# Kernel tuning notes

Measured on AMD Instinct MI355X. Metric: run time of the kernel, lower is better.

Reference implementation:

```python
import jax, jax.numpy as jnp
import numpy as np

N_NODES = 50000
N_EDGES = 800000
IN_C, HID_C, LAT_C = 128, 64, 32
DEC_HID, REC_C = 64, 128


def _glorot(key, shape):
    fan_in, fan_out = shape
    lim = jnp.sqrt(6.0 / (fan_in + fan_out))
    return jax.random.uniform(key, shape, jnp.float32, -lim, lim)


def setup_inputs() -> dict:
    key = jax.random.key(0)
    ks = jax.random.split(key, 8)
    x = jax.random.normal(ks[0], (N_NODES, IN_C), jnp.float32)
    edge_index = jax.random.randint(ks[1], (2, N_EDGES), 0, N_NODES, jnp.int64 if jax.config.jax_enable_x64 else jnp.int32)
    return {
        "x": x,
        "edge_index": edge_index,
        "W_e1": _glorot(ks[2], (IN_C, HID_C)), "b_e1": jnp.zeros((HID_C,), jnp.float32),
        "W_e2": _glorot(ks[3], (HID_C, LAT_C)), "b_e2": jnp.zeros((LAT_C,), jnp.float32),
        "W_d1": _glorot(ks[4], (LAT_C, DEC_HID)), "b_d1": jnp.zeros((DEC_HID,), jnp.float32),
        "W_d2": _glorot(ks[5], (DEC_HID, REC_C)), "b_d2": jnp.zeros((REC_C,), jnp.float32),
    }


def _gcn_conv(x, src, dst, dinv, W, b, n_nodes):
    # GCNConv: h = D^{-1/2} (A + I) D^{-1/2} (x W) + b, expressed over the edge list
    h = x @ W                                   # [N, out]
    norm = dinv[src] * dinv[dst]                # [E+N] symmetric normalization
    msg = h[src] * norm[:, None]                # gather + per-edge scale (memory-bound)
    out = jax.ops.segment_sum(msg, dst, num_segments=n_nodes)  # scatter-add
    return out + b


def reference(x, edge_index, W_e1, b_e1, W_e2, b_e2, W_d1, b_d1, W_d2, b_d2):
    n = x.shape[0]
    loops = jnp.arange(n, dtype=edge_index.dtype)
    src = jnp.concatenate([edge_index[0], loops])
    dst = jnp.concatenate([edge_index[1], loops])
    # degree (with self-loops) computed once; deg >= 1 so rsqrt is safe
    deg = jax.ops.segment_sum(jnp.ones_like(src, dtype=x.dtype), dst, num_segments=n)
    dinv = jax.lax.rsqrt(deg)

    # encoder (dropout is eval-mode identity)
    h = jax.nn.relu(_gcn_conv(x, src, dst, dinv, W_e1, b_e1, n))
    z = _gcn_conv(h, src, dst, dinv, W_e2, b_e2, n)           # latent embeddings
    # decoder mirrors GCNConv layers
    d = jax.nn.relu(_gcn_conv(z, src, dst, dinv, W_d1, b_d1, n))
    x_rec = _gcn_conv(d, src, dst, dinv, W_d2, b_d2, n)       # [N, reconstructed_feature_dim]
    return x_rec
```

## Files before the change

kernel.cpp:

```cpp
#include <hip/hip_runtime.h>

typedef _Float16 half4 __attribute__((ext_vector_type(4)));


static constexpr int NPB_SHIFT = 6;
static constexpr int NPB = 1 << NPB_SHIFT;
static constexpr int MAX_BKT = 1024;
static constexpr int PS_CHUNK = 4096;

__global__ __launch_bounds__(256) void hist_kernel(const int* __restrict__ dst, int E,
                                                   int nbkt, int* __restrict__ hist) {
    __shared__ int lc[MAX_BKT];
    int tid = threadIdx.x;
    int b = blockIdx.x;
    int e0 = b * PS_CHUNK;
    int e1 = e0 + PS_CHUNK; if (e1 > E) e1 = E;
    for (int i = tid; i < nbkt; i += 256) lc[i] = 0;
    __syncthreads();
    for (int i = e0 + tid; i < e1; i += 256)
        atomicAdd(&lc[dst[i] >> NPB_SHIFT], 1);
    __syncthreads();
    for (int i = tid; i < nbkt; i += 256) hist[(size_t)b * nbkt + i] = lc[i];
}

__global__ __launch_bounds__(256) void col_scan_kernel(int* __restrict__ hist, int nchunk,
                                                       int nbkt, int* __restrict__ bcnt) {
    int i = blockIdx.x * 4 + (threadIdx.x >> 6);
    if (i >= nbkt) return;
    int lane = threadIdx.x & 63;
    int run = 0;
    for (int c0 = 0; c0 < nchunk; c0 += 64) {
        int c = c0 + lane;
        int v = (c < nchunk) ? hist[(size_t)c * nbkt + i] : 0;
        int inc = v;
#pragma unroll
        for (int m = 1; m < 64; m <<= 1) {
            int u = __shfl_up(inc, m);
            if (lane >= m) inc += u;
        }
        if (c < nchunk) hist[(size_t)c * nbkt + i] = run + inc - v;
        run += __shfl(inc, 63);
    }
    if (lane == 0) bcnt[i] = run;
}

__global__ __launch_bounds__(256) void bucket_scan_kernel(const int* __restrict__ bcnt, int nbkt,
                                                          int* __restrict__ bbase,
                                                          int* __restrict__ rowp, int n) {
    __shared__ int wsum[4];
    int tid = threadIdx.x, lane = tid & 63, w = tid >> 6;
    int chunk = (nbkt + 255) / 256;
    int begin = tid * chunk;
    int end = begin + chunk; if (end > nbkt) end = nbkt;
    int s = 0;
    for (int i = begin; i < end; ++i) s += bcnt[i];
    int inc = s;
#pragma unroll
    for (int m = 1; m < 64; m <<= 1) {
        int u = __shfl_up(inc, m);
        if (lane >= m) inc += u;
    }
    if (lane == 63) wsum[w] = inc;
    __syncthreads();
    int off = 0;
    for (int i = 0; i < w; ++i) off += wsum[i];
    int run = off + inc - s;
    for (int i = begin; i < end; ++i) {
        bbase[i] = run;
        run += bcnt[i];
    }
    if (tid == 255) { bbase[nbkt] = run; rowp[n] = run; }
}

__global__ __launch_bounds__(256) void pair_blocksort_kernel(const int* __restrict__ src,
                                                             const int* __restrict__ dst,
                                                             int E, int nbkt,
                                                             const int* __restrict__ hist,
                                                             const int* __restrict__ bbase,
                                                             int2* __restrict__ part) {
    __shared__ int2 pairs[PS_CHUNK];
    __shared__ int lbase[MAX_BKT];
    __shared__ int lcur[MAX_BKT];
    __shared__ int gpos[MAX_BKT];
    __shared__ int wsum[4];
    const int tid = threadIdx.x;
    const int b = blockIdx.x;
    const int e0 = b * PS_CHUNK;
    int e1 = e0 + PS_CHUNK; if (e1 > E) e1 = E;

    for (int i = tid; i < nbkt; i += 256) {
        lcur[i] = 0;
        gpos[i] = bbase[i] + hist[(size_t)b * nbkt + i];
    }
    __syncthreads();
    for (int i = e0 + tid; i < e1; i += 256)
        atomicAdd(&lcur[dst[i] >> NPB_SHIFT], 1);
    __syncthreads();
    {
        int b0 = tid * 4;
        int v[4]; int s = 0;
#pragma unroll
        for (int k = 0; k < 4; ++k) {
            int bb = b0 + k;
            v[k] = (bb < nbkt) ? lcur[bb] : 0;
            s += v[k];
        }
        int lane = tid & 63, w = tid >> 6;
        int inc = s;
#pragma unroll
        for (int m = 1; m < 64; m <<= 1) {
            int u = __shfl_up(inc, m);
            if (lane >= m) inc += u;
        }
        if (lane == 63) wsum[w] = inc;
        __syncthreads();
        int off = 0;
        for (int i = 0; i < w; ++i) off += wsum[i];
        int run = off + inc - s;
        __syncthreads();
#pragma unroll
        for (int k = 0; k < 4; ++k) {
            int bb = b0 + k;
            if (bb < nbkt) { lbase[bb] = run; lcur[bb] = run; }
            run += v[k];
        }
    }
    __syncthreads();
    for (int i = e0 + tid; i < e1; i += 256) {
        int s = src[i], d = dst[i];
        int p = atomicAdd(&lcur[d >> NPB_SHIFT], 1);
        pairs[p] = make_int2(s, d);
    }
    __syncthreads();
    const int cnt = e1 - e0;
    for (int i = tid; i < cnt; i += 256) {
        int2 pr = pairs[i];
        int bk = pr.y >> NPB_SHIFT;
        part[gpos[bk] + (i - lbase[bk])] = pr;
    }
}

__global__ __launch_bounds__(256) void bucket_csr_kernel(const int2* __restrict__ part,
                                                         const int* __restrict__ bbase, int n,
                                                         int* __restrict__ rowp,
                                                         float* __restrict__ dinv,
                                                         int* __restrict__ csr) {
    __shared__ int lcnt[NPB];
    int b = blockIdx.x, tid = threadIdx.x;
    int node0 = b << NPB_SHIFT;
    int nloc = n - node0; if (nloc > NPB) nloc = NPB;
    int p0 = bbase[b], p1 = bbase[b + 1];
    if (tid < NPB) lcnt[tid] = 0;
    __syncthreads();
    for (int i = p0 + tid; i < p1; i += 256)
        atomicAdd(&lcnt[part[i].y & (NPB - 1)], 1);
    __syncthreads();
    if (tid < 64) {
        int c = lcnt[tid];
        int inc = c;
#pragma unroll
        for (int m = 1; m < 64; m <<= 1) {
            int u = __shfl_up(inc, m);
            if (tid >= m) inc += u;
        }
        int base = p0 + inc - c;
        if (tid < nloc) {
            rowp[node0 + tid] = base;
            dinv[node0 + tid] = rsqrtf((float)(c + 1));
        }
        lcnt[tid] = base;
    }
    __syncthreads();
    for (int i = p0 + tid; i < p1; i += 256) {
        int2 pr = part[i];
        int pos = atomicAdd(&lcnt[pr.y & (NPB - 1)], 1);
        csr[pos] = pr.x;
    }
}


template <bool HALF>
__device__ __forceinline__ float4 ldrow4(const void* H, size_t off) {
    if constexpr (HALF) {
        half4 h = *reinterpret_cast<const half4*>(reinterpret_cast<const _Float16*>(H) + off);
        return make_float4((float)h.x, (float)h.y, (float)h.z, (float)h.w);
    } else {
        return *reinterpret_cast<const float4*>(reinterpret_cast<const float*>(H) + off);
    }
}

template <bool HALF>
__device__ __forceinline__ void strow4(void* H, size_t off, float4 o) {
    if constexpr (HALF) {
        half4 hv;
        hv.x = (_Float16)o.x; hv.y = (_Float16)o.y;
        hv.z = (_Float16)o.z; hv.w = (_Float16)o.w;
        *reinterpret_cast<half4*>(reinterpret_cast<_Float16*>(H) + off) = hv;
    } else {
        *reinterpret_cast<float4*>(reinterpret_cast<float*>(H) + off) = o;
    }
}

template <int K, int OUT, int BN, bool BIAS, bool RELU, bool SCALE, bool HALF_IN, bool HALF_OUT>
__global__ __launch_bounds__(16 * (BN / 4)) void gemm_tile_kernel(
        const void* __restrict__ X, const float* __restrict__ W,
        const float* __restrict__ bias, const float* __restrict__ dinv,
        void* __restrict__ Hout, int n) {
    constexpr int BM = 64;
    constexpr int KB = (K > 64) ? 64 : K;
    constexpr int NTHR = 16 * (BN / 4);
    constexpr int KV = KB / 4;

    __shared__ float At[KB][BM + 4];
    __shared__ float Bl[K][BN];

    const int tid = threadIdx.x;
    const int tx = tid % (BN / 4);
    const int ty = tid / (BN / 4);
    const int rb = blockIdx.x * BM;
    const int co = blockIdx.y * BN;

    for (int i = tid; i < K * BN / 4; i += NTHR) {
        int k = i / (BN / 4);
        int c0 = (i % (BN / 4)) * 4;
        *reinterpret_cast<float4*>(&Bl[k][c0]) =
            *reinterpret_cast<const float4*>(&W[(size_t)k * OUT + co + c0]);
    }

    float acc[4][4] = {};

#pragma unroll
    for (int ch = 0; ch < K / KB; ++ch) {
        if (ch) __syncthreads();
        for (int i = tid; i < BM * KV; i += NTHR) {
            int r = i / KV;
            int k0 = (i % KV) * 4;
            int rg = rb + r; if (rg > n - 1) rg = n - 1;
            float4 xv = ldrow4<HALF_IN>(X, (size_t)rg * K + ch * KB + k0);
            At[k0 + 0][r] = xv.x;
            At[k0 + 1][r] = xv.y;
            At[k0 + 2][r] = xv.z;
            At[k0 + 3][r] = xv.w;
        }
        __syncthreads();

#pragma unroll 8
        for (int k = 0; k < KB; ++k) {
            float4 a = *reinterpret_cast<const float4*>(&At[k][ty * 4]);
            float4 b = *reinterpret_cast<const float4*>(&Bl[ch * KB + k][tx * 4]);
            acc[0][0] = fmaf(a.x, b.x, acc[0][0]); acc[0][1] = fmaf(a.x, b.y, acc[0][1]);
            acc[0][2] = fmaf(a.x, b.z, acc[0][2]); acc[0][3] = fmaf(a.x, b.w, acc[0][3]);
            acc[1][0] = fmaf(a.y, b.x, acc[1][0]); acc[1][1] = fmaf(a.y, b.y, acc[1][1]);
            acc[1][2] = fmaf(a.y, b.z, acc[1][2]); acc[1][3] = fmaf(a.y, b.w, acc[1][3]);
            acc[2][0] = fmaf(a.z, b.x, acc[2][0]); acc[2][1] = fmaf(a.z, b.y, acc[2][1]);
            acc[2][2] = fmaf(a.z, b.z, acc[2][2]); acc[2][3] = fmaf(a.z, b.w, acc[2][3]);
            acc[3][0] = fmaf(a.w, b.x, acc[3][0]); acc[3][1] = fmaf(a.w, b.y, acc[3][1]);
            acc[3][2] = fmaf(a.w, b.z, acc[3][2]); acc[3][3] = fmaf(a.w, b.w, acc[3][3]);
        }
    }

    float4 bv = make_float4(0.f, 0.f, 0.f, 0.f);
    if (BIAS) bv = *reinterpret_cast<const float4*>(&bias[co + tx * 4]);
    int r0 = rb + ty * 4;
#pragma unroll
    for (int i = 0; i < 4; ++i) {
        int r = r0 + i;
        if (r < n) {
            float4 o;
            o.x = acc[i][0]; o.y = acc[i][1]; o.z = acc[i][2]; o.w = acc[i][3];
            if (BIAS) { o.x += bv.x; o.y += bv.y; o.z += bv.z; o.w += bv.w; }
            if (RELU) {
                o.x = fmaxf(o.x, 0.f); o.y = fmaxf(o.y, 0.f);
                o.z = fmaxf(o.z, 0.f); o.w = fmaxf(o.w, 0.f);
            }
            if (SCALE) {
                float dv = dinv[r];
                o.x *= dv; o.y *= dv; o.z *= dv; o.w *= dv;
            }
            strow4<HALF_OUT>(Hout, (size_t)r * OUT + co + tx * 4, o);
        }
    }
}

template <int C, bool RELU, bool HAS_BIAS, bool POST_SCALE, bool HALF_IN, bool HALF_OUT>
__global__ __launch_bounds__(256) void aggregate_kernel(const void* __restrict__ H,
                                                        const int* __restrict__ row,
                                                        const int* __restrict__ csr_src,
                                                        const float* __restrict__ dinv,
                                                        const float* __restrict__ bias,
                                                        void* __restrict__ Y, int n) {
    constexpr int LPN = C / 4;
    constexpr int EG = 64 / LPN;
    int wid = (blockIdx.x * blockDim.x + threadIdx.x) >> 6;
    if (wid >= n) return;
    int lane = threadIdx.x & 63;
    int g = lane / LPN;
    int c0 = (lane % LPN) * 4;
    const int node = wid;

    float4 a0 = make_float4(0.f, 0.f, 0.f, 0.f);
    float4 a1 = a0, a2 = a0, a3 = a0;
    if (g == 0) a0 = ldrow4<HALF_IN>(H, (size_t)node * C + c0);
    int e = row[node] + g;
    int end = row[node + 1];
    for (; e + 3 * EG < end; e += 4 * EG) {
        int s0 = csr_src[e];
        int s1 = csr_src[e + EG];
        int s2 = csr_src[e + 2 * EG];
        int s3 = csr_src[e + 3 * EG];
        float4 h0 = ldrow4<HALF_IN>(H, (size_t)s0 * C + c0);
        float4 h1 = ldrow4<HALF_IN>(H, (size_t)s1 * C + c0);
        float4 h2 = ldrow4<HALF_IN>(H, (size_t)s2 * C + c0);
        float4 h3 = ldrow4<HALF_IN>(H, (size_t)s3 * C + c0);
        a0.x += h0.x; a0.y += h0.y; a0.z += h0.z; a0.w += h0.w;
        a1.x += h1.x; a1.y += h1.y; a1.z += h1.z; a1.w += h1.w;
        a2.x += h2.x; a2.y += h2.y; a2.z += h2.z; a2.w += h2.w;
        a3.x += h3.x; a3.y += h3.y; a3.z += h3.z; a3.w += h3.w;
    }
    for (; e < end; e += EG) {
        int s = csr_src[e];
        float4 hv = ldrow4<HALF_IN>(H, (size_t)s * C + c0);
        a0.x += hv.x; a0.y += hv.y; a0.z += hv.z; a0.w += hv.w;
    }
    float4 acc;
    acc.x = (a0.x + a1.x) + (a2.x + a3.x);
    acc.y = (a0.y + a1.y) + (a2.y + a3.y);
    acc.z = (a0.z + a1.z) + (a2.z + a3.z);
    acc.w = (a0.w + a1.w) + (a2.w + a3.w);
#pragma unroll
    for (int m = LPN; m < 64; m <<= 1) {
        acc.x += __shfl_xor(acc.x, m);
        acc.y += __shfl_xor(acc.y, m);
        acc.z += __shfl_xor(acc.z, m);
        acc.w += __shfl_xor(acc.w, m);
    }
    if (g == 0) {
        float dv = dinv[node];
        float4 o;
        o.x = acc.x * dv; o.y = acc.y * dv; o.z = acc.z * dv; o.w = acc.w * dv;
        if (HAS_BIAS) {
            o.x += bias[c0 + 0]; o.y += bias[c0 + 1];
            o.z += bias[c0 + 2]; o.w += bias[c0 + 3];
        }
        if (RELU) {
            o.x = fmaxf(o.x, 0.f); o.y = fmaxf(o.y, 0.f);
            o.z = fmaxf(o.z, 0.f); o.w = fmaxf(o.w, 0.f);
        }
        if (POST_SCALE) { o.x *= dv; o.y *= dv; o.z *= dv; o.w *= dv; }
        strow4<HALF_OUT>(Y, (size_t)node * C + c0, o);
    }
}


static inline int cdiv(int a, int b) { return (a + b - 1) / b; }

extern "C" void kernel_launch(void* const* d_in, const int* in_sizes, int n_in,
                              void* d_out, int out_size, void* d_ws, size_t ws_size,
                              hipStream_t stream) {
    const float* x   = (const float*)d_in[0];
    const int*   ei  = (const int*)d_in[1];
    const float* We1 = (const float*)d_in[2];
    const float* be1 = (const float*)d_in[3];
    const float* We2 = (const float*)d_in[4];
    const float* be2 = (const float*)d_in[5];
    const float* Wd1 = (const float*)d_in[6];
    const float* bd1 = (const float*)d_in[7];
    const float* Wd2 = (const float*)d_in[8];
    const float* bd2 = (const float*)d_in[9];

    const int n = in_sizes[0] / 128;
    const int E = in_sizes[1] / 2;
    const int* src = ei;
    const int* dst = ei + E;
    const int nbkt = cdiv(n, NPB);
    const int nchunk = cdiv(E, PS_CHUNK);
    const int nrb = cdiv(n, 64);
    const int nwv = cdiv(n * 64, 256);

    char* ws = (char*)d_ws;
    auto carve = [&](size_t bytes) -> void* {
        void* p = (void*)ws;
        ws += (bytes + 255) & ~(size_t)255;
        return p;
    };
    int*   hist = (int*)carve((size_t)nchunk * nbkt * 4);
    int*   bcnt = (int*)carve((size_t)nbkt * 4);
    int*   bbase= (int*)carve((size_t)(nbkt + 1) * 4);
    int2*  part = (int2*)carve((size_t)E * 8);
    int*   rowp = (int*)carve((size_t)(n + 1) * 4);
    float* dinv = (float*)carve((size_t)n * 4);
    int*   csr  = (int*)carve((size_t)E * 4);
    void*  bufA = carve((size_t)n * 64 * 4);
    void*  bufB = carve((size_t)n * 64 * 4);
    void*  bufC = carve((size_t)n * 32 * 4);

    hist_kernel<<<nchunk, 256, 0, stream>>>(dst, E, nbkt, hist);
    col_scan_kernel<<<cdiv(nbkt, 4), 256, 0, stream>>>(hist, nchunk, nbkt, bcnt);
    bucket_scan_kernel<<<1, 256, 0, stream>>>(bcnt, nbkt, bbase, rowp, n);
    pair_blocksort_kernel<<<nchunk, 256, 0, stream>>>(src, dst, E, nbkt, hist, bbase, part);
    bucket_csr_kernel<<<nbkt, 256, 0, stream>>>(part, bbase, n, rowp, dinv, csr);

    gemm_tile_kernel<128, 64, 64, false, false, true, false, true>
        <<<dim3(nrb, 1), 256, 0, stream>>>(x, We1, nullptr, dinv, bufA, n);
    aggregate_kernel<64, true, true, false, true, true>
        <<<nwv, 256, 0, stream>>>(bufA, rowp, csr, dinv, be1, bufB, n);

    gemm_tile_kernel<64, 32, 32, false, false, true, true, true>
        <<<dim3(nrb, 1), 128, 0, stream>>>(bufB, We2, nullptr, dinv, bufA, n);
    aggregate_kernel<32, false, true, true, true, true>
        <<<nwv, 256, 0, stream>>>(bufA, rowp, csr, dinv, be2, bufC, n);

    aggregate_kernel<32, false, false, false, true, true>
        <<<nwv, 256, 0, stream>>>(bufC, rowp, csr, dinv, nullptr, bufA, n);
    gemm_tile_kernel<32, 64, 64, true, true, true, true, true>
        <<<dim3(nrb, 1), 256, 0, stream>>>(bufA, Wd1, bd1, dinv, bufB, n);

    aggregate_kernel<64, false, false, false, true, true>
        <<<nwv, 256, 0, stream>>>(bufB, rowp, csr, dinv, nullptr, bufA, n);
    gemm_tile_kernel<64, 128, 64, true, false, false, true, false>
        <<<dim3(nrb, 2), 256, 0, stream>>>(bufA, Wd2, bd2, dinv, d_out, n);
}
```

Baseline: 197.9 us.

## Fuse CSR build with first GEMM and aggregation with following GEMMs

Packs each (src,dst) pair into a single int, which halves the partition buffer. The bucket CSR build is merged with the first-layer GEMM, since a 64-node bucket matches a 64-row GEMM tile. Three aggregate-then-GEMM pairs become one agg_gemm kernel: aggregated rows are staged in fp16 shared memory and multiplied by a shared-memory fp16 copy of W. This removes kernel launches and intermediate global round trips. In exchange, the fused kernels have large shared-memory footprints, which may lower occupancy, and the weights are rounded to fp16.

```diff
diff --git a/kernel.cpp b/kernel.cpp
--- a/kernel.cpp
+++ b/kernel.cpp
@@ -77,7 +77,7 @@
                                                              int E, int nbkt,
                                                              const int* __restrict__ hist,
                                                              const int* __restrict__ bbase,
-                                                             int2* __restrict__ part) {
+                                                             int* __restrict__ part) {
     __shared__ int2 pairs[PS_CHUNK];
     __shared__ int lbase[MAX_BKT];
     __shared__ int lcur[MAX_BKT];
@@ -136,45 +136,7 @@
     for (int i = tid; i < cnt; i += 256) {
         int2 pr = pairs[i];
         int bk = pr.y >> NPB_SHIFT;
-        part[gpos[bk] + (i - lbase[bk])] = pr;
-    }
-}
-
-__global__ __launch_bounds__(256) void bucket_csr_kernel(const int2* __restrict__ part,
-                                                         const int* __restrict__ bbase, int n,
-                                                         int* __restrict__ rowp,
-                                                         float* __restrict__ dinv,
-                                                         int* __restrict__ csr) {
-    __shared__ int lcnt[NPB];
-    int b = blockIdx.x, tid = threadIdx.x;
-    int node0 = b << NPB_SHIFT;
-    int nloc = n - node0; if (nloc > NPB) nloc = NPB;
-    int p0 = bbase[b], p1 = bbase[b + 1];
-    if (tid < NPB) lcnt[tid] = 0;
-    __syncthreads();
-    for (int i = p0 + tid; i < p1; i += 256)
-        atomicAdd(&lcnt[part[i].y & (NPB - 1)], 1);
-    __syncthreads();
-    if (tid < 64) {
-        int c = lcnt[tid];
-        int inc = c;
-#pragma unroll
-        for (int m = 1; m < 64; m <<= 1) {
-            int u = __shfl_up(inc, m);
-            if (tid >= m) inc += u;
-        }
-        int base = p0 + inc - c;
-        if (tid < nloc) {
-            rowp[node0 + tid] = base;
-            dinv[node0 + tid] = rsqrtf((float)(c + 1));
-        }
-        lcnt[tid] = base;
-    }
-    __syncthreads();
-    for (int i = p0 + tid; i < p1; i += 256) {
-        int2 pr = part[i];
-        int pos = atomicAdd(&lcnt[pr.y & (NPB - 1)], 1);
-        csr[pos] = pr.x;
+        part[gpos[bk] + (i - lbase[bk])] = (pr.x << NPB_SHIFT) | (pr.y & (NPB - 1));
     }
 }
 
@@ -201,84 +163,213 @@
     }
 }
 
-template <int K, int OUT, int BN, bool BIAS, bool RELU, bool SCALE, bool HALF_IN, bool HALF_OUT>
-__global__ __launch_bounds__(16 * (BN / 4)) void gemm_tile_kernel(
-        const void* __restrict__ X, const float* __restrict__ W,
-        const float* __restrict__ bias, const float* __restrict__ dinv,
-        void* __restrict__ Hout, int n) {
-    constexpr int BM = 64;
-    constexpr int KB = (K > 64) ? 64 : K;
-    constexpr int NTHR = 16 * (BN / 4);
-    constexpr int KV = KB / 4;
-
-    __shared__ float At[KB][BM + 4];
-    __shared__ float Bl[K][BN];
-
-    const int tid = threadIdx.x;
-    const int tx = tid % (BN / 4);
-    const int ty = tid / (BN / 4);
-    const int rb = blockIdx.x * BM;
-    const int co = blockIdx.y * BN;
-
-    for (int i = tid; i < K * BN / 4; i += NTHR) {
-        int k = i / (BN / 4);
-        int c0 = (i % (BN / 4)) * 4;
-        *reinterpret_cast<float4*>(&Bl[k][c0]) =
-            *reinterpret_cast<const float4*>(&W[(size_t)k * OUT + co + c0]);
+__global__ __launch_bounds__(256) void csr_g1_kernel(
+        const int* __restrict__ part, const int* __restrict__ bbase, int n,
+        int* __restrict__ rowp, float* __restrict__ dinv, int* __restrict__ csr,
+        const float* __restrict__ X, const float* __restrict__ We1,
+        void* __restrict__ H1) {
+    __shared__ int lcnt[NPB];
+    __shared__ float sdinv[NPB];
+    __shared__ __align__(16) char smem[50176];
+    const int b = blockIdx.x, tid = threadIdx.x;
+    const int node0 = b << NPB_SHIFT;
+    int nloc = n - node0; if (nloc > NPB) nloc = NPB;
+    const int p0 = bbase[b], p1 = bbase[b + 1];
+
+    if (tid < NPB) lcnt[tid] = 0;
+    __syncthreads();
+    for (int i = p0 + tid; i < p1; i += 256)
+        atomicAdd(&lcnt[part[i] & (NPB - 1)], 1);
+    __syncthreads();
+    if (tid < 64) {
+        int c = lcnt[tid];
+        int inc = c;
+#pragma unroll
+        for (int m = 1; m < 64; m <<= 1) {
+            int u = __shfl_up(inc, m);
+            if (tid >= m) inc += u;
+        }
+        int base = p0 + inc - c;
+        float dv = rsqrtf((float)(c + 1));
+        if (tid < nloc) {
+            rowp[node0 + tid] = base;
+            dinv[node0 + tid] = dv;
+        }
+        sdinv[tid] = dv;
+        lcnt[tid] = base;
+    }
+    __syncthreads();
+    for (int i = p0 + tid; i < p1; i += 256) {
+        int w = part[i];
+        int pos = atomicAdd(&lcnt[w & (NPB - 1)], 1);
+        csr[pos] = w >> NPB_SHIFT;
+    }
+    __syncthreads();
+
+    float (*At)[68] = reinterpret_cast<float (*)[68]>(smem);
+    float (*Bl)[64] = reinterpret_cast<float (*)[64]>(smem + 17408);
+    const int tx = tid % 16, ty = tid / 16;
+
+    for (int i = tid; i < 128 * 16; i += 256) {
+        int k = i / 16, c4 = (i % 16) * 4;
+        *reinterpret_cast<float4*>(&Bl[k][c4]) =
+            *reinterpret_cast<const float4*>(&We1[(size_t)k * 64 + c4]);
     }
 
     float acc[4][4] = {};
-
-#pragma unroll
-    for (int ch = 0; ch < K / KB; ++ch) {
+#pragma unroll
+    for (int ch = 0; ch < 2; ++ch) {
         if (ch) __syncthreads();
-        for (int i = tid; i < BM * KV; i += NTHR) {
-            int r = i / KV;
-            int k0 = (i % KV) * 4;
-            int rg = rb + r; if (rg > n - 1) rg = n - 1;
-            float4 xv = ldrow4<HALF_IN>(X, (size_t)rg * K + ch * KB + k0);
+        for (int i = tid; i < 64 * 16; i += 256) {
+            int r = i / 16, k0 = (i % 16) * 4;
+            int rg = node0 + r; if (rg > n - 1) rg = n - 1;
+            float4 xv = *reinterpret_cast<const float4*>(&X[(size_t)rg * 128 + ch * 64 + k0]);
             At[k0 + 0][r] = xv.x;
             At[k0 + 1][r] = xv.y;
             At[k0 + 2][r] = xv.z;
             At[k0 + 3][r] = xv.w;
         }
         __syncthreads();
-
 #pragma unroll 8
-        for (int k = 0; k < KB; ++k) {
+        for (int k = 0; k < 64; ++k) {
             float4 a = *reinterpret_cast<const float4*>(&At[k][ty * 4]);
-            float4 b = *reinterpret_cast<const float4*>(&Bl[ch * KB + k][tx * 4]);
-            acc[0][0] = fmaf(a.x, b.x, acc[0][0]); acc[0][1] = fmaf(a.x, b.y, acc[0][1]);
-            acc[0][2] = fmaf(a.x, b.z, acc[0][2]); acc[0][3] = fmaf(a.x, b.w, acc[0][3]);
-            acc[1][0] = fmaf(a.y, b.x, acc[1][0]); acc[1][1] = fmaf(a.y, b.y, acc[1][1]);
-            acc[1][2] = fmaf(a.y, b.z, acc[1][2]); acc[1][3] = fmaf(a.y, b.w, acc[1][3]);
-            acc[2][0] = fmaf(a.z, b.x, acc[2][0]); acc[2][1] = fmaf(a.z, b.y, acc[2][1]);
-            acc[2][2] = fmaf(a.z, b.z, acc[2][2]); acc[2][3] = fmaf(a.z, b.w, acc[2][3]);
-            acc[3][0] = fmaf(a.w, b.x, acc[3][0]); acc[3][1] = fmaf(a.w, b.y, acc[3][1]);
-            acc[3][2] = fmaf(a.w, b.z, acc[3][2]); acc[3][3] = fmaf(a.w, b.w, acc[3][3]);
-        }
-    }
-
-    float4 bv = make_float4(0.f, 0.f, 0.f, 0.f);
-    if (BIAS) bv = *reinterpret_cast<const float4*>(&bias[co + tx * 4]);
-    int r0 = rb + ty * 4;
+            float4 bb = *reinterpret_cast<const float4*>(&Bl[ch * 64 + k][tx * 4]);
+            acc[0][0] = fmaf(a.x, bb.x, acc[0][0]); acc[0][1] = fmaf(a.x, bb.y, acc[0][1]);
+            acc[0][2] = fmaf(a.x, bb.z, acc[0][2]); acc[0][3] = fmaf(a.x, bb.w, acc[0][3]);
+            acc[1][0] = fmaf(a.y, bb.x, acc[1][0]); acc[1][1] = fmaf(a.y, bb.y, acc[1][1]);
+            acc[1][2] = fmaf(a.y, bb.z, acc[1][2]); acc[1][3] = fmaf(a.y, bb.w, acc[1][3]);
+            acc[2][0] = fmaf(a.z, bb.x, acc[2][0]); acc[2][1] = fmaf(a.z, bb.y, acc[2][1]);
+            acc[2][2] = fmaf(a.z, bb.z, acc[2][2]); acc[2][3] = fmaf(a.z, bb.w, acc[2][3]);
+            acc[3][0] = fmaf(a.w, bb.x, acc[3][0]); acc[3][1] = fmaf(a.w, bb.y, acc[3][1]);
+            acc[3][2] = fmaf(a.w, bb.z, acc[3][2]); acc[3][3] = fmaf(a.w, bb.w, acc[3][3]);
+        }
+    }
 #pragma unroll
     for (int i = 0; i < 4; ++i) {
-        int r = r0 + i;
-        if (r < n) {
-            float4 o;
-            o.x = acc[i][0]; o.y = acc[i][1]; o.z = acc[i][2]; o.w = acc[i][3];
-            if (BIAS) { o.x += bv.x; o.y += bv.y; o.z += bv.z; o.w += bv.w; }
-            if (RELU) {
-                o.x = fmaxf(o.x, 0.f); o.y = fmaxf(o.y, 0.f);
-                o.z = fmaxf(o.z, 0.f); o.w = fmaxf(o.w, 0.f);
+        int r = ty * 4 + i;
+        int nd = node0 + r;
+        if (nd < n) {
+            float dv = sdinv[r];
+            float4 o = make_float4(acc[i][0] * dv, acc[i][1] * dv,
+                                   acc[i][2] * dv, acc[i][3] * dv);
+            strow4<true>(H1, (size_t)nd * 64 + tx * 4, o);
+        }
+    }
+}
+
+template <int CIN, int COUT, bool A_BIAS, bool A_RELU,
+          bool B_BIAS, bool B_RELU, bool B_SCALE, bool OUT_HALF>
+__global__ __launch_bounds__(256) void agg_gemm_kernel(
+        const void* __restrict__ H, const int* __restrict__ rowp,
+        const int* __restrict__ csr, const float* __restrict__ dinv,
+        const float* __restrict__ abias, const float* __restrict__ W,
+        const float* __restrict__ bbias, void* __restrict__ Out, int n) {
+    constexpr int ROWS = 32;
+    constexpr int HSTR = CIN + 12;
+    constexpr int LPN = CIN / 4;
+    constexpr int EG = 64 / LPN;
+    __shared__ _Float16 Ht[ROWS][HSTR];
+    __shared__ _Float16 Wl[CIN][COUT];
+    __shared__ float sdinv[ROWS];
+    const int tid = threadIdx.x;
+    const int node0 = blockIdx.x * ROWS;
+
+    for (int i = tid; i < CIN * COUT; i += 256)
+        Wl[i / COUT][i % COUT] = (_Float16)W[i];
+
+    const int wv = tid >> 6, lane = tid & 63;
+    const int g = lane / LPN;
+    const int c0 = (lane % LPN) * 4;
+
+    for (int it = 0; it < ROWS / 4; ++it) {
+        const int rl = wv * (ROWS / 4) + it;
+        const int nd = node0 + rl;
+        if (nd < n) {
+            float4 a0 = make_float4(0.f, 0.f, 0.f, 0.f);
+            float4 a1 = a0, a2 = a0, a3 = a0;
+            if (g == 0) a0 = ldrow4<true>(H, (size_t)nd * CIN + c0);
+            int e = rowp[nd] + g;
+            const int end = rowp[nd + 1];
+            for (; e + 3 * EG < end; e += 4 * EG) {
+                int s0 = csr[e];
+                int s1 = csr[e + EG];
+                int s2 = csr[e + 2 * EG];
+                int s3 = csr[e + 3 * EG];
+                float4 h0 = ldrow4<true>(H, (size_t)s0 * CIN + c0);
+                float4 h1 = ldrow4<true>(H, (size_t)s1 * CIN + c0);
+                float4 h2 = ldrow4<true>(H, (size_t)s2 * CIN + c0);
+                float4 h3 = ldrow4<true>(H, (size_t)s3 * CIN + c0);
+                a0.x += h0.x; a0.y += h0.y; a0.z += h0.z; a0.w += h0.w;
+                a1.x += h1.x; a1.y += h1.y; a1.z += h1.z; a1.w += h1.w;
+                a2.x += h2.x; a2.y += h2.y; a2.z += h2.z; a2.w += h2.w;
+                a3.x += h3.x; a3.y += h3.y; a3.z += h3.z; a3.w += h3.w;
             }
-            if (SCALE) {
-                float dv = dinv[r];
-                o.x *= dv; o.y *= dv; o.z *= dv; o.w *= dv;
+            for (; e < end; e += EG) {
+                int s = csr[e];
+                float4 hv = ldrow4<true>(H, (size_t)s * CIN + c0);
+                a0.x += hv.x; a0.y += hv.y; a0.z += hv.z; a0.w += hv.w;
             }
-            strow4<HALF_OUT>(Hout, (size_t)r * OUT + co + tx * 4, o);
-        }
+            float4 acc;
+            acc.x = (a0.x + a1.x) + (a2.x + a3.x);
+            acc.y = (a0.y + a1.y) + (a2.y + a3.y);
+            acc.z = (a0.z + a1.z) + (a2.z + a3.z);
+            acc.w = (a0.w + a1.w) + (a2.w + a3.w);
+#pragma unroll
+            for (int m = LPN; m < 64; m <<= 1) {
+                acc.x += __shfl_xor(acc.x, m);
+                acc.y += __shfl_xor(acc.y, m);
+                acc.z += __shfl_xor(acc.z, m);
+                acc.w += __shfl_xor(acc.w, m);
+            }
+            if (g == 0) {
+                float dv = dinv[nd];
+                float4 o = make_float4(acc.x * dv, acc.y * dv, acc.z * dv, acc.w * dv);
+                if constexpr (A_BIAS) {
+                    o.x += abias[c0 + 0]; o.y += abias[c0 + 1];
+                    o.z += abias[c0 + 2]; o.w += abias[c0 + 3];
+                }
+                if constexpr (A_RELU) {
+                    o.x = fmaxf(o.x, 0.f); o.y = fmaxf(o.y, 0.f);
+                    o.z = fmaxf(o.z, 0.f); o.w = fmaxf(o.w, 0.f);
+                }
+                half4 hv;
+                hv.x = (_Float16)o.x; hv.y = (_Float16)o.y;
+                hv.z = (_Float16)o.z; hv.w = (_Float16)o.w;
+                *reinterpret_cast<half4*>(&Ht[rl][c0]) = hv;
+                if (lane == 0) sdinv[rl] = dv;
+            }
+        }
+    }
+    __syncthreads();
+
+    constexpr int CG = COUT / 4;
+    for (int o4 = tid; o4 < ROWS * CG; o4 += 256) {
+        int r = o4 / CG, cg = o4 % CG;
+        int nd = node0 + r;
+        if (nd >= n) continue;
+        float4 acc = make_float4(0.f, 0.f, 0.f, 0.f);
+#pragma unroll 8
+        for (int k = 0; k < CIN; ++k) {
+            float a = (float)Ht[r][k];
+            half4 w4 = *reinterpret_cast<const half4*>(&Wl[k][cg * 4]);
+            acc.x = fmaf(a, (float)w4.x, acc.x);
+            acc.y = fmaf(a, (float)w4.y, acc.y);
+            acc.z = fmaf(a, (float)w4.z, acc.z);
+            acc.w = fmaf(a, (float)w4.w, acc.w);
+        }
+        if constexpr (B_BIAS) {
+            acc.x += bbias[cg * 4 + 0]; acc.y += bbias[cg * 4 + 1];
+            acc.z += bbias[cg * 4 + 2]; acc.w += bbias[cg * 4 + 3];
+        }
+        if constexpr (B_RELU) {
+            acc.x = fmaxf(acc.x, 0.f); acc.y = fmaxf(acc.y, 0.f);
+            acc.z = fmaxf(acc.z, 0.f); acc.w = fmaxf(acc.w, 0.f);
+        }
+        if constexpr (B_SCALE) {
+            float dv = sdinv[r];
+            acc.x *= dv; acc.y *= dv; acc.z *= dv; acc.w *= dv;
+        }
+        strow4<OUT_HALF>(Out, (size_t)nd * COUT + cg * 4, acc);
     }
 }
 
@@ -374,7 +465,7 @@
     const int* dst = ei + E;
     const int nbkt = cdiv(n, NPB);
     const int nchunk = cdiv(E, PS_CHUNK);
-    const int nrb = cdiv(n, 64);
+    const int nag = cdiv(n, 32);
     const int nwv = cdiv(n * 64, 256);
 
     char* ws = (char*)d_ws;
@@ -386,37 +477,30 @@
     int*   hist = (int*)carve((size_t)nchunk * nbkt * 4);
     int*   bcnt = (int*)carve((size_t)nbkt * 4);
     int*   bbase= (int*)carve((size_t)(nbkt + 1) * 4);
-    int2*  part = (int2*)carve((size_t)E * 8);
+    int*   part = (int*)carve((size_t)E * 4);
     int*   rowp = (int*)carve((size_t)(n + 1) * 4);
     float* dinv = (float*)carve((size_t)n * 4);
     int*   csr  = (int*)carve((size_t)E * 4);
-    void*  bufA = carve((size_t)n * 64 * 4);
-    void*  bufB = carve((size_t)n * 64 * 4);
-    void*  bufC = carve((size_t)n * 32 * 4);
+    void*  bufA = carve((size_t)n * 64 * 2);
+    void*  bufB = carve((size_t)n * 32 * 2);
+    void*  bufC = carve((size_t)n * 32 * 2);
 
     hist_kernel<<<nchunk, 256, 0, stream>>>(dst, E, nbkt, hist);
     col_scan_kernel<<<cdiv(nbkt, 4), 256, 0, stream>>>(hist, nchunk, nbkt, bcnt);
     bucket_scan_kernel<<<1, 256, 0, stream>>>(bcnt, nbkt, bbase, rowp, n);
     pair_blocksort_kernel<<<nchunk, 256, 0, stream>>>(src, dst, E, nbkt, hist, bbase, part);
-    bucket_csr_kernel<<<nbkt, 256, 0, stream>>>(part, bbase, n, rowp, dinv, csr);
-
-    gemm_tile_kernel<128, 64, 64, false, false, true, false, true>
-        <<<dim3(nrb, 1), 256, 0, stream>>>(x, We1, nullptr, dinv, bufA, n);
-    aggregate_kernel<64, true, true, false, true, true>
-        <<<nwv, 256, 0, stream>>>(bufA, rowp, csr, dinv, be1, bufB, n);
-
-    gemm_tile_kernel<64, 32, 32, false, false, true, true, true>
-        <<<dim3(nrb, 1), 128, 0, stream>>>(bufB, We2, nullptr, dinv, bufA, n);
+
+    csr_g1_kernel<<<nbkt, 256, 0, stream>>>(part, bbase, n, rowp, dinv, csr, x, We1, bufA);
+
+    agg_gemm_kernel<64, 32, true, true, false, false, true, true>
+        <<<nag, 256, 0, stream>>>(bufA, rowp, csr, dinv, be1, We2, nullptr, bufB, n);
+
     aggregate_kernel<32, false, true, true, true, true>
-        <<<nwv, 256, 0, stream>>>(bufA, rowp, csr, dinv, be2, bufC, n);
-
-    aggregate_kernel<32, false, false, false, true, true>
-        <<<nwv, 256, 0, stream>>>(bufC, rowp, csr, dinv, nullptr, bufA, n);
-    gemm_tile_kernel<32, 64, 64, true, true, true, true, true>
-        <<<dim3(nrb, 1), 256, 0, stream>>>(bufA, Wd1, bd1, dinv, bufB, n);
-
-    aggregate_kernel<64, false, false, false, true, true>
-        <<<nwv, 256, 0, stream>>>(bufB, rowp, csr, dinv, nullptr, bufA, n);
-    gemm_tile_kernel<64, 128, 64, true, false, false, true, false>
-        <<<dim3(nrb, 2), 256, 0, stream>>>(bufA, Wd2, bd2, dinv, d_out, n);
-}
+        <<<nwv, 256, 0, stream>>>(bufB, rowp, csr, dinv, be2, bufC, n);
+
+    agg_gemm_kernel<32, 64, false, false, true, true, true, true>
+        <<<nag, 256, 0, stream>>>(bufC, rowp, csr, dinv, nullptr, Wd1, bd1, bufA, n);
+
+    agg_gemm_kernel<64, 128, false, false, true, false, false, false>
+        <<<nag, 256, 0, stream>>>(bufA, rowp, csr, dinv, nullptr, Wd2, bd2, d_out, n);
+}
```

Measured after the change: 203.1 us. 1.03x slower.

## Fuse CSR build with first GEMM, pack edge pairs, split wide aggregations

Applied to the files above, without the earlier changes.

The bucket CSR kernel and the first encoder GEMM are merged into one kernel per 64-node bucket, which reuses the degree normalization from shared memory and saves a launch and a dinv reload. Edge pairs are packed into a single int (src<<6 | local dst), halving the partition buffer traffic. The 64-channel aggregations now split each node across two wavefronts (two 32-channel slices) to raise parallelism, and intermediate buffers are resized to fp16. In exchange, the fused kernel uses about 50KB of shared memory, which may lower occupancy. The packing also assumes src << 6 fits in an int, which holds for this node count.

```diff
diff --git a/kernel.cpp b/kernel.cpp
--- a/kernel.cpp
+++ b/kernel.cpp
@@ -77,7 +77,7 @@
                                                              int E, int nbkt,
                                                              const int* __restrict__ hist,
                                                              const int* __restrict__ bbase,
-                                                             int2* __restrict__ part) {
+                                                             int* __restrict__ part) {
     __shared__ int2 pairs[PS_CHUNK];
     __shared__ int lbase[MAX_BKT];
     __shared__ int lcur[MAX_BKT];
@@ -136,45 +136,7 @@
     for (int i = tid; i < cnt; i += 256) {
         int2 pr = pairs[i];
         int bk = pr.y >> NPB_SHIFT;
-        part[gpos[bk] + (i - lbase[bk])] = pr;
-    }
-}
-
-__global__ __launch_bounds__(256) void bucket_csr_kernel(const int2* __restrict__ part,
-                                                         const int* __restrict__ bbase, int n,
-                                                         int* __restrict__ rowp,
-                                                         float* __restrict__ dinv,
-                                                         int* __restrict__ csr) {
-    __shared__ int lcnt[NPB];
-    int b = blockIdx.x, tid = threadIdx.x;
-    int node0 = b << NPB_SHIFT;
-    int nloc = n - node0; if (nloc > NPB) nloc = NPB;
-    int p0 = bbase[b], p1 = bbase[b + 1];
-    if (tid < NPB) lcnt[tid] = 0;
-    __syncthreads();
-    for (int i = p0 + tid; i < p1; i += 256)
-        atomicAdd(&lcnt[part[i].y & (NPB - 1)], 1);
-    __syncthreads();
-    if (tid < 64) {
-        int c = lcnt[tid];
-        int inc = c;
-#pragma unroll
-        for (int m = 1; m < 64; m <<= 1) {
-            int u = __shfl_up(inc, m);
-            if (tid >= m) inc += u;
-        }
-        int base = p0 + inc - c;
-        if (tid < nloc) {
-            rowp[node0 + tid] = base;
-            dinv[node0 + tid] = rsqrtf((float)(c + 1));
-        }
-        lcnt[tid] = base;
-    }
-    __syncthreads();
-    for (int i = p0 + tid; i < p1; i += 256) {
-        int2 pr = part[i];
-        int pos = atomicAdd(&lcnt[pr.y & (NPB - 1)], 1);
-        csr[pos] = pr.x;
+        part[gpos[bk] + (i - lbase[bk])] = (pr.x << NPB_SHIFT) | (pr.y & (NPB - 1));
     }
 }
 
@@ -198,6 +160,100 @@
         *reinterpret_cast<half4*>(reinterpret_cast<_Float16*>(H) + off) = hv;
     } else {
         *reinterpret_cast<float4*>(reinterpret_cast<float*>(H) + off) = o;
+    }
+}
+
+__global__ __launch_bounds__(256) void csr_g1_kernel(
+        const int* __restrict__ part, const int* __restrict__ bbase, int n,
+        int* __restrict__ rowp, float* __restrict__ dinv, int* __restrict__ csr,
+        const float* __restrict__ X, const float* __restrict__ We1,
+        void* __restrict__ H1) {
+    __shared__ int lcnt[NPB];
+    __shared__ float sdinv[NPB];
+    __shared__ __align__(16) char smem[50176];
+    const int b = blockIdx.x, tid = threadIdx.x;
+    const int node0 = b << NPB_SHIFT;
+    int nloc = n - node0; if (nloc > NPB) nloc = NPB;
+    const int p0 = bbase[b], p1 = bbase[b + 1];
+
+    if (tid < NPB) lcnt[tid] = 0;
+    __syncthreads();
+    for (int i = p0 + tid; i < p1; i += 256)
+        atomicAdd(&lcnt[part[i] & (NPB - 1)], 1);
+    __syncthreads();
+    if (tid < 64) {
+        int c = lcnt[tid];
+        int inc = c;
+#pragma unroll
+        for (int m = 1; m < 64; m <<= 1) {
+            int u = __shfl_up(inc, m);
+            if (tid >= m) inc += u;
+        }
+        int base = p0 + inc - c;
+        float dv = rsqrtf((float)(c + 1));
+        if (tid < nloc) {
+            rowp[node0 + tid] = base;
+            dinv[node0 + tid] = dv;
+        }
+        sdinv[tid] = dv;
+        lcnt[tid] = base;
+    }
+    __syncthreads();
+    for (int i = p0 + tid; i < p1; i += 256) {
+        int w = part[i];
+        int pos = atomicAdd(&lcnt[w & (NPB - 1)], 1);
+        csr[pos] = w >> NPB_SHIFT;
+    }
+    __syncthreads();
+
+    float (*At)[68] = reinterpret_cast<float (*)[68]>(smem);
+    float (*Bl)[64] = reinterpret_cast<float (*)[64]>(smem + 17408);
+    const int tx = tid % 16, ty = tid / 16;
+
+    for (int i = tid; i < 128 * 16; i += 256) {
+        int k = i / 16, c4 = (i % 16) * 4;
+        *reinterpret_cast<float4*>(&Bl[k][c4]) =
+            *reinterpret_cast<const float4*>(&We1[(size_t)k * 64 + c4]);
+    }
+
+    float acc[4][4] = {};
+#pragma unroll
+    for (int ch = 0; ch < 2; ++ch) {
+        if (ch) __syncthreads();
+        for (int i = tid; i < 64 * 16; i += 256) {
+            int r = i / 16, k0 = (i % 16) * 4;
+            int rg = node0 + r; if (rg > n - 1) rg = n - 1;
+            float4 xv = *reinterpret_cast<const float4*>(&X[(size_t)rg * 128 + ch * 64 + k0]);
+            At[k0 + 0][r] = xv.x;
+            At[k0 + 1][r] = xv.y;
+            At[k0 + 2][r] = xv.z;
+            At[k0 + 3][r] = xv.w;
+        }
+        __syncthreads();
+#pragma unroll 8
+        for (int k = 0; k < 64; ++k) {
+            float4 a = *reinterpret_cast<const float4*>(&At[k][ty * 4]);
+            float4 bb = *reinterpret_cast<const float4*>(&Bl[ch * 64 + k][tx * 4]);
+            acc[0][0] = fmaf(a.x, bb.x, acc[0][0]); acc[0][1] = fmaf(a.x, bb.y, acc[0][1]);
+            acc[0][2] = fmaf(a.x, bb.z, acc[0][2]); acc[0][3] = fmaf(a.x, bb.w, acc[0][3]);
+            acc[1][0] = fmaf(a.y, bb.x, acc[1][0]); acc[1][1] = fmaf(a.y, bb.y, acc[1][1]);
+            acc[1][2] = fmaf(a.y, bb.z, acc[1][2]); acc[1][3] = fmaf(a.y, bb.w, acc[1][3]);
+            acc[2][0] = fmaf(a.z, bb.x, acc[2][0]); acc[2][1] = fmaf(a.z, bb.y, acc[2][1]);
+            acc[2][2] = fmaf(a.z, bb.z, acc[2][2]); acc[2][3] = fmaf(a.z, bb.w, acc[2][3]);
+            acc[3][0] = fmaf(a.w, bb.x, acc[3][0]); acc[3][1] = fmaf(a.w, bb.y, acc[3][1]);
+            acc[3][2] = fmaf(a.w, bb.z, acc[3][2]); acc[3][3] = fmaf(a.w, bb.w, acc[3][3]);
+        }
+    }
+#pragma unroll
+    for (int i = 0; i < 4; ++i) {
+        int r = ty * 4 + i;
+        int nd = node0 + r;
+        if (nd < n) {
+            float dv = sdinv[r];
+            float4 o = make_float4(acc[i][0] * dv, acc[i][1] * dv,
+                                   acc[i][2] * dv, acc[i][3] * dv);
+            strow4<true>(H1, (size_t)nd * 64 + tx * 4, o);
+        }
     }
 }
 
@@ -282,21 +338,23 @@
     }
 }
 
-template <int C, bool RELU, bool HAS_BIAS, bool POST_SCALE, bool HALF_IN, bool HALF_OUT>
+template <int C, int SLICES, bool RELU, bool HAS_BIAS, bool POST_SCALE, bool HALF_IN, bool HALF_OUT>
 __global__ __launch_bounds__(256) void aggregate_kernel(const void* __restrict__ H,
                                                         const int* __restrict__ row,
                                                         const int* __restrict__ csr_src,
                                                         const float* __restrict__ dinv,
                                                         const float* __restrict__ bias,
                                                         void* __restrict__ Y, int n) {
-    constexpr int LPN = C / 4;
+    constexpr int CS = C / SLICES;
+    constexpr int LPN = CS / 4;
     constexpr int EG = 64 / LPN;
     int wid = (blockIdx.x * blockDim.x + threadIdx.x) >> 6;
-    if (wid >= n) return;
+    if (wid >= n * SLICES) return;
+    const int node = (SLICES > 1) ? (wid >> 1) : wid;
+    const int slice = (SLICES > 1) ? (wid & 1) : 0;
     int lane = threadIdx.x & 63;
     int g = lane / LPN;
-    int c0 = (lane % LPN) * 4;
-    const int node = wid;
+    int c0 = slice * CS + (lane % LPN) * 4;
 
     float4 a0 = make_float4(0.f, 0.f, 0.f, 0.f);
     float4 a1 = a0, a2 = a0, a3 = a0;
@@ -375,7 +433,8 @@
     const int nbkt = cdiv(n, NPB);
     const int nchunk = cdiv(E, PS_CHUNK);
     const int nrb = cdiv(n, 64);
-    const int nwv = cdiv(n * 64, 256);
+    const int nwv1 = cdiv(n * 64, 256);
+    const int nwv2 = cdiv(n * 2 * 64, 256);
 
     char* ws = (char*)d_ws;
     auto carve = [&](size_t bytes) -> void* {
@@ -386,37 +445,40 @@
     int*   hist = (int*)carve((size_t)nchunk * nbkt * 4);
     int*   bcnt = (int*)carve((size_t)nbkt * 4);
     int*   bbase= (int*)carve((size_t)(nbkt + 1) * 4);
-    int2*  part = (int2*)carve((size_t)E * 8);
+    int*   part = (int*)carve((size_t)E * 4);
     int*   rowp = (int*)carve((size_t)(n + 1) * 4);
     float* dinv = (float*)carve((size_t)n * 4);
     int*   csr  = (int*)carve((size_t)E * 4);
-    void*  bufA = carve((size_t)n * 64 * 4);
-    void*  bufB = carve((size_t)n * 64 * 4);
-    void*  bufC = carve((size_t)n * 32 * 4);
+    void*  P1 = carve((size_t)n * 64 * 2);
+    void*  P2 = carve((size_t)n * 64 * 2);
+    void*  P3 = carve((size_t)n * 32 * 2);
+    void*  P4 = carve((size_t)n * 32 * 2);
 
     hist_kernel<<<nchunk, 256, 0, stream>>>(dst, E, nbkt, hist);
     col_scan_kernel<<<cdiv(nbkt, 4), 256, 0, stream>>>(hist, nchunk, nbkt, bcnt);
     bucket_scan_kernel<<<1, 256, 0, stream>>>(bcnt, nbkt, bbase, rowp, n);
     pair_blocksort_kernel<<<nchunk, 256, 0, stream>>>(src, dst, E, nbkt, hist, bbase, part);
-    bucket_csr_kernel<<<nbkt, 256, 0, stream>>>(part, bbase, n, rowp, dinv, csr);
-
-    gemm_tile_kernel<128, 64, 64, false, false, true, false, true>
-        <<<dim3(nrb, 1), 256, 0, stream>>>(x, We1, nullptr, dinv, bufA, n);
-    aggregate_kernel<64, true, true, false, true, true>
-        <<<nwv, 256, 0, stream>>>(bufA, rowp, csr, dinv, be1, bufB, n);
+
+    csr_g1_kernel<<<nbkt, 256, 0, stream>>>(part, bbase, n, rowp, dinv, csr, x, We1, P1);
+
+    aggregate_kernel<64, 2, true, true, false, true, true>
+        <<<nwv2, 256, 0, stream>>>(P1, rowp, csr, dinv, be1, P2, n);
 
     gemm_tile_kernel<64, 32, 32, false, false, true, true, true>
-        <<<dim3(nrb, 1), 128, 0, stream>>>(bufB, We2, nullptr, dinv, bufA, n);
-    aggregate_kernel<32, false, true, true, true, true>
-        <<<nwv, 256, 0, stream>>>(bufA, rowp, csr, dinv, be2, bufC, n);
-
-    aggregate_kernel<32, false, false, false, true, true>
-        <<<nwv, 256, 0, stream>>>(bufC, rowp, csr, dinv, nullptr, bufA, n);
+        <<<dim3(nrb, 1), 128, 0, stream>>>(P2, We2, nullptr, dinv, P3, n);
+
+    aggregate_kernel<32, 1, false, true, true, true, true>
+        <<<nwv1, 256, 0, stream>>>(P3, rowp, csr, dinv, be2, P4, n);
+
+    aggregate_kernel<32, 1, false, false, false, true, true>
+        <<<nwv1, 256, 0, stream>>>(P4, rowp, csr, dinv, nullptr, P3, n);
+
     gemm_tile_kernel<32, 64, 64, true, true, true, true, true>
-        <<<dim3(nrb, 1), 256, 0, stream>>>(bufA, Wd1, bd1, dinv, bufB, n);
-
-    aggregate_kernel<64, false, false, false, true, true>
-        <<<nwv, 256, 0, stream>>>(bufB, rowp, csr, dinv, nullptr, bufA, n);
+        <<<dim3(nrb, 1), 256, 0, stream>>>(P3, Wd1, bd1, dinv, P1, n);
+
+    aggregate_kernel<64, 2, false, false, false, true, true>
+        <<<nwv2, 256, 0, stream>>>(P1, rowp, csr, dinv, nullptr, P2, n);
+
     gemm_tile_kernel<64, 128, 64, true, false, false, true, false>
-        <<<dim3(nrb, 2), 256, 0, stream>>>(bufA, Wd2, bd2, dinv, d_out, n);
-}
+        <<<dim3(nrb, 2), 256, 0, stream>>>(P2, Wd2, bd2, dinv, d_out, n);
+}
```

Measured after the change: 219.9 us. +11.1%, slower.
